# Optimization experiments

Hardware: AMD Instinct MI355X
Metric: run time of the kernel (lower is better)

Reference implementation:

```python
import jax, jax.numpy as jnp
import numpy as np

B, L, D = 2, 2048, 2048
NUM_HEADS = 32
KV_GROUPS = 8
GROUP_SIZE = NUM_HEADS // KV_GROUPS  # 4
HEAD_DIM = D // NUM_HEADS            # 64


def _rope_tables(L, hd):
    # standard RoPE angle tables, duplicated across halves to width hd
    inv_freq = 1.0 / (10000.0 ** (np.arange(0, hd, 2, dtype=np.float32) / hd))
    ang = np.arange(L, dtype=np.float32)[:, None] * inv_freq[None, :]  # [L, hd/2]
    cos = np.concatenate([np.cos(ang), np.cos(ang)], axis=-1)
    sin = np.concatenate([np.sin(ang), np.sin(ang)], axis=-1)
    return jnp.asarray(cos), jnp.asarray(sin)


def setup_inputs() -> dict:
    key = jax.random.key(0)
    ks = jax.random.split(key, 6)
    x = jax.random.normal(ks[0], (B, L, D), dtype=jnp.float32)
    mask = jnp.triu(jnp.ones((L, L), dtype=bool), k=1)  # causal: True above diag
    cos, sin = _rope_tables(L, HEAD_DIM)
    s = 0.02
    Wq = jax.random.normal(ks[1], (D, D), dtype=jnp.float32) * s
    Wk = jax.random.normal(ks[2], (D, KV_GROUPS * HEAD_DIM), dtype=jnp.float32) * s
    Wv = jax.random.normal(ks[3], (D, KV_GROUPS * HEAD_DIM), dtype=jnp.float32) * s
    Wo = jax.random.normal(ks[4], (D, D), dtype=jnp.float32) * s
    bo = jnp.zeros((D,), dtype=jnp.float32)
    return {"x": x, "mask": mask, "cos": cos, "sin": sin,
            "Wq": Wq, "Wk": Wk, "Wv": Wv, "Wo": Wo, "bo": bo}


def _apply_rope(t, cos, sin):
    # t: [B, H, L, hd]
    hd = t.shape[-1]
    t1, t2 = t[..., : hd // 2], t[..., hd // 2:]
    rotated = jnp.concatenate([-t2, t1], axis=-1)
    return t * cos[None, None, :, :] + rotated * sin[None, None, :, :]


def reference(x, mask, cos, sin, Wq, Wk, Wv, Wo, bo):
    Bv, Lv, Dv = x.shape
    hd = HEAD_DIM
    q = (x @ Wq).reshape(Bv, Lv, NUM_HEADS, hd).transpose(0, 2, 1, 3)   # [B,H,L,hd]
    k = (x @ Wk).reshape(Bv, Lv, KV_GROUPS, hd).transpose(0, 2, 1, 3)   # [B,G,L,hd]
    v = (x @ Wv).reshape(Bv, Lv, KV_GROUPS, hd).transpose(0, 2, 1, 3)
    q = _apply_rope(q, cos, sin)
    k = _apply_rope(k, cos, sin)
    k = jnp.repeat(k, GROUP_SIZE, axis=1)  # [B,H,L,hd]
    v = jnp.repeat(v, GROUP_SIZE, axis=1)
    scores = jnp.einsum('bhqd,bhkd->bhqk', q, k) / jnp.sqrt(jnp.float32(hd))
    scores = jnp.where(mask[None, None, :, :], -jnp.inf, scores)
    attn = jax.nn.softmax(scores, axis=-1)
    out = jnp.einsum('bhqk,bhkd->bhqd', attn, v)         # [B,H,L,hd]
    out = out.transpose(0, 2, 1, 3).reshape(Bv, Lv, Dv)  # [B,L,D]
    return out @ Wo + bo
```

## Files before the change

kernel.cpp:

```cpp
#include <hip/hip_runtime.h>
#include <cstdint>

typedef unsigned short UST;
typedef __bf16 v8bf __attribute__((ext_vector_type(8)));
typedef float v4f __attribute__((ext_vector_type(4)));

static __device__ __forceinline__ UST f2b(float f) {
  union { float f; uint32_t u; } c; c.f = f;
  uint32_t u = c.u;
  u += 0x7fffu + ((u >> 16) & 1u);
  return (UST)(u >> 16);
}
static __device__ __forceinline__ float b2f(UST h) {
  union { uint32_t u; float f; } c; c.u = ((uint32_t)h) << 16;
  return c.f;
}
static __device__ __forceinline__ uint32_t cvtpk(float lo, float hi) {
  uint32_t r;
  asm("v_cvt_pk_bf16_f32 %0, %1, %2" : "=v"(r) : "v"(lo), "v"(hi));
  return r;
}
static __device__ __forceinline__ float fexp2(float x) {
  float r;
  asm("v_exp_f32 %0, %1" : "=v"(r) : "v"(x));
  return r;
}
template <int N>
static __device__ __forceinline__ void wait_vm() {
  asm volatile("s_waitcnt vmcnt(%0)" :: "i"(N));
}

static __device__ __forceinline__ void gl_lds16(const UST* g, UST* l) {
  __builtin_amdgcn_global_load_lds(
      (const __attribute__((address_space(1))) void*)g,
      (__attribute__((address_space(3))) void*)l, 16, 0, 0);
}

__global__ __launch_bounds__(256) void k_cast(const float* __restrict__ src,
                                              UST* __restrict__ dst) {
  size_t i = (size_t)blockIdx.x * 256 + threadIdx.x;
  const float4* s4 = reinterpret_cast<const float4*>(src) + 2 * i;
  float4 a = s4[0], b = s4[1];
  union { UST s[8]; uint4 v; } r;
  r.s[0] = f2b(a.x); r.s[1] = f2b(a.y); r.s[2] = f2b(a.z); r.s[3] = f2b(a.w);
  r.s[4] = f2b(b.x); r.s[5] = f2b(b.y); r.s[6] = f2b(b.z); r.s[7] = f2b(b.w);
  reinterpret_cast<uint4*>(dst)[i] = r.v;
}

__global__ __launch_bounds__(256) void k_castT(const float* __restrict__ W,
                                               UST* __restrict__ dst, int N, int K) {
  __shared__ float tile[32][33];
  int nt = blockIdx.x * 32, kt = blockIdx.y * 32;
  int tx = threadIdx.x, ty = threadIdx.y;
#pragma unroll
  for (int r = 0; r < 4; ++r)
    tile[ty + r * 8][tx] = W[(size_t)(kt + ty + r * 8) * N + nt + tx];
  __syncthreads();
#pragma unroll
  for (int r = 0; r < 4; ++r)
    dst[(size_t)(nt + ty + r * 8) * K + kt + tx] = f2b(tile[tx][ty + r * 8]);
}

template <int BM, int BN, int WM, int WN, int EPI>
__global__ __launch_bounds__(512, 2) void k_gemm2(const UST* __restrict__ A,
                                                  const UST* __restrict__ Bt,
                                                  void* __restrict__ Cv,
                                                  const float* __restrict__ bias,
                                                  int M, int N, int K, int ntn) {
  constexpr int WMR = BM / WM, WNR = BN / WN;
  constexpr int MF = WMR / 16, NF = WNR / 16;
  constexpr int CA = BM / 64, CB = BN / 64;
  constexpr int NKEEP = CA + CB;
  constexpr int AE = 2 * BM * 64;
  __shared__ __align__(16) UST lds[AE + 2 * BN * 64];

  int tid = threadIdx.x, w = tid >> 6, lane = tid & 63;
  int lr = lane & 15, lg = lane >> 4;
  int wm = w / WN, wn = w % WN;

  int q = (int)gridDim.x >> 3;
  int bid = (int)blockIdx.x;
  int swz = (bid & 7) * q + (bid >> 3);
  int mBlk = (swz / ntn) * BM, nBlk = (swz % ntn) * BN;

  v4f acc[MF][NF];
#pragma unroll
  for (int i = 0; i < MF; ++i)
#pragma unroll
    for (int j = 0; j < NF; ++j) acc[i][j] = (v4f){0.f, 0.f, 0.f, 0.f};

  int tr = tid >> 3;
  int sg = (tid & 7) ^ (tr & 7);
  const UST* AbL = A + (size_t)(mBlk + tr) * K + sg * 8;
  const UST* BbL = Bt + (size_t)(nBlk + tr) * K + sg * 8;
  int ldsW = w * 512;

  auto stageA = [&](int bf, int kt) {
#pragma unroll
    for (int c = 0; c < CA; ++c)
      gl_lds16(AbL + (size_t)(c * 64) * K + kt * 64,
               &lds[bf * BM * 64 + c * 4096 + ldsW]);
  };
  auto stageB = [&](int bf, int kt) {
#pragma unroll
    for (int c = 0; c < CB; ++c)
      gl_lds16(BbL + (size_t)(c * 64) * K + kt * 64,
               &lds[AE + bf * BN * 64 + c * 4096 + ldsW]);
  };
  auto ldA = [&](int bf, int s, int f) -> v8bf {
    int row = wm * WMR + f * 16 + lr;
    return *(const v8bf*)&lds[(bf * BM + row) * 64 + (((s * 4 + lg) ^ (lr & 7)) * 8)];
  };
  auto ldB = [&](int bf, int s, int nf) -> v8bf {
    int row = wn * WNR + nf * 16 + lr;
    return *(const v8bf*)&lds[AE + (bf * BN + row) * 64 + (((s * 4 + lg) ^ (lr & 7)) * 8)];
  };

  int NT = K >> 6;
  stageA(0, 0); stageB(0, 0);

  for (int kt = 0; kt < NT; ++kt) {
    int bf = kt & 1, nb = bf ^ 1;
    if (kt + 1 < NT) {
      stageA(nb, kt + 1); stageB(nb, kt + 1);
      wait_vm<NKEEP>();
    } else {
      wait_vm<0>();
    }
    __syncthreads();
#pragma unroll
    for (int s = 0; s < 2; ++s) {
      v8bf afr[MF], bfr[NF];
#pragma unroll
      for (int nf = 0; nf < NF; ++nf) bfr[nf] = ldB(bf, s, nf);
#pragma unroll
      for (int f = 0; f < MF; ++f) afr[f] = ldA(bf, s, f);
      __builtin_amdgcn_s_setprio(1);
#pragma unroll
      for (int f = 0; f < MF; ++f)
#pragma unroll
        for (int nf = 0; nf < NF; ++nf)
          acc[f][nf] = __builtin_amdgcn_mfma_f32_16x16x32_bf16(
              afr[f], bfr[nf], acc[f][nf], 0, 0, 0);
      __builtin_amdgcn_s_setprio(0);
    }
    __syncthreads();
  }

  int row0 = mBlk + wm * WMR + lg * 4;
  int col0 = nBlk + wn * WNR + lr;
#pragma unroll
  for (int fm = 0; fm < MF; ++fm)
#pragma unroll
    for (int nf = 0; nf < NF; ++nf)
#pragma unroll
      for (int r = 0; r < 4; ++r) {
        int row = row0 + fm * 16 + r;
        int col = col0 + nf * 16;
        if constexpr (EPI == 0) {
          ((UST*)Cv)[(size_t)row * N + col] = f2b(acc[fm][nf][r]);
        } else {
          ((float*)Cv)[(size_t)row * N + col] = acc[fm][nf][r] + bias[col];
        }
      }
}

__global__ __launch_bounds__(256) void k_rope(const UST* __restrict__ qkv,
                                              const float* __restrict__ cosT,
                                              const float* __restrict__ sinT,
                                              UST* __restrict__ qh,
                                              UST* __restrict__ kh) {
  int idx = blockIdx.x * 256 + threadIdx.x;
  int d = idx & 31;
  int hh = (idx >> 5) % 40;
  int row = idx / 1280;
  int l = row & 2047, b = row >> 11;
  int col = (hh < 32) ? hh * 64 : 2048 + (hh - 32) * 64;
  float t1 = b2f(qkv[(size_t)row * 3072 + col + d]);
  float t2 = b2f(qkv[(size_t)row * 3072 + col + d + 32]);
  float c = cosT[l * 64 + d], s = sinT[l * 64 + d];
  float o1 = t1 * c - t2 * s;
  float o2 = t2 * c + t1 * s;
  if (hh < 32) {
    size_t base = (((size_t)b * 32 + hh) * 2048 + l) * 64 + d;
    qh[base] = f2b(o1 * 0.125f);
    qh[base + 32] = f2b(o2 * 0.125f);
  } else {
    size_t base = (((size_t)b * 8 + (hh - 32)) * 2048 + l) * 64 + d;
    kh[base] = f2b(o1);
    kh[base + 32] = f2b(o2);
  }
}

__global__ __launch_bounds__(256) void k_vtrans(const UST* __restrict__ qkv,
                                                UST* __restrict__ vt) {
  __shared__ __align__(16) UST tl[64][72];
  int lt = blockIdx.x, bg = blockIdx.y;
  int b = bg >> 3, g = bg & 7;
  int t = threadIdx.x;
  int li = t >> 2, d0 = (t & 3) * 16;
  const UST* src = qkv + (size_t)(b * 2048 + lt * 64 + li) * 3072 + 2560 + g * 64 + d0;
  *(uint4*)&tl[li][d0] = *(const uint4*)src;
  *(uint4*)&tl[li][d0 + 8] = *(const uint4*)(src + 8);
  __syncthreads();
  int d = t >> 2, l0 = (t & 3) * 16;
  union { UST u[8]; uint4 v; } r0, r1;
#pragma unroll
  for (int e = 0; e < 8; ++e) r0.u[e] = tl[l0 + e][d];
#pragma unroll
  for (int e = 0; e < 8; ++e) r1.u[e] = tl[l0 + 8 + e][d];
  UST* dstp = vt + (size_t)((b * 8 + g) * 64 + d) * 2048 + (size_t)lt * 64 + l0;
  *(uint4*)dstp = r0.v;
  *(uint4*)(dstp + 8) = r1.v;
}

__global__ __launch_bounds__(512, 4) void k_attn(const UST* __restrict__ qh,
                                                 const UST* __restrict__ kh,
                                                 const UST* __restrict__ vt,
                                                 UST* __restrict__ outp) {
  __shared__ __align__(16) UST k_s[128 * 72];
  __shared__ __align__(16) UST v_s[64 * 136];
  __shared__ __align__(16) UST p_s[8][16 * 136];
  int bx = blockIdx.x, h = blockIdx.y, b = blockIdx.z;
  int g = h >> 2;
  int tid = threadIdx.x, w = tid >> 6, lane = tid & 63;
  int lr = lane & 15, lg = lane >> 4;

  int ksr = tid >> 2, ksc = (tid & 3) * 16;
  int vsr = tid >> 3, vsc = (tid & 7) * 16;
  const UST* kbase = kh + ((size_t)(b * 8 + g) * 2048 + ksr) * 64 + ksc;
  const UST* vbase = vt + ((size_t)(b * 8 + g) * 64 + vsr) * 2048 + vsc;
  UST* kdst = &k_s[ksr * 72 + ksc];
  UST* vdst = &v_s[vsr * 136 + vsc];

  for (int half = 0; half < 2; ++half) {
    int qt = half ? (15 - bx) : bx;
    int qbase = qt * 128 + w * 16;

    const UST* qp = qh + ((size_t)(b * 32 + h) * 2048 + qbase + lr) * 64 + lg * 8;
    v8bf qf0 = *(const v8bf*)qp;
    v8bf qf1 = *(const v8bf*)(qp + 32);

    float m = -1e30f, ls = 0.f;
    v4f o[4];
#pragma unroll
    for (int dt = 0; dt < 4; ++dt) o[dt] = (v4f){0.f, 0.f, 0.f, 0.f};

    __syncthreads();
    uint4 pk0 = *(const uint4*)kbase, pk1 = *(const uint4*)(kbase + 8);
    uint4 pv0 = *(const uint4*)vbase, pv1 = *(const uint4*)(vbase + 8);
    *(uint4*)kdst = pk0; *(uint4*)(kdst + 8) = pk1;
    *(uint4*)vdst = pv0; *(uint4*)(vdst + 8) = pv1;

    for (int j = 0; j <= qt; ++j) {
      __syncthreads();
      bool pref = (j < qt);
      if (pref) {
        const UST* kg = kbase + (size_t)(j + 1) * 8192;
        const UST* vg = vbase + (j + 1) * 128;
        pk0 = *(const uint4*)kg; pk1 = *(const uint4*)(kg + 8);
        pv0 = *(const uint4*)vg; pv1 = *(const uint4*)(vg + 8);
      }

      v4f st[8];
      __builtin_amdgcn_s_setprio(1);
#pragma unroll
      for (int kt = 0; kt < 8; ++kt) {
        const UST* kr = &k_s[(kt * 16 + lr) * 72 + lg * 8];
        v8bf kf0 = *(const v8bf*)kr;
        v8bf kf1 = *(const v8bf*)(kr + 32);
        v4f z = (v4f){0.f, 0.f, 0.f, 0.f};
        z = __builtin_amdgcn_mfma_f32_16x16x32_bf16(kf0, qf0, z, 0, 0, 0);
        z = __builtin_amdgcn_mfma_f32_16x16x32_bf16(kf1, qf1, z, 0, 0, 0);
        st[kt] = z;
      }
      __builtin_amdgcn_s_setprio(0);
      if (j == qt) {
        int qg = qbase + lr;
#pragma unroll
        for (int kt = 0; kt < 8; ++kt)
#pragma unroll
          for (int r = 0; r < 4; ++r) {
            int kg2 = j * 128 + kt * 16 + 4 * lg + r;
            if (kg2 > qg) st[kt][r] = -1e30f;
          }
      }

      float t0 = fmaxf(fmaxf(st[0][0], st[0][1]), fmaxf(st[0][2], st[0][3]));
      float t1 = fmaxf(fmaxf(st[1][0], st[1][1]), fmaxf(st[1][2], st[1][3]));
      float t2 = fmaxf(fmaxf(st[2][0], st[2][1]), fmaxf(st[2][2], st[2][3]));
      float t3 = fmaxf(fmaxf(st[3][0], st[3][1]), fmaxf(st[3][2], st[3][3]));
      float t4 = fmaxf(fmaxf(st[4][0], st[4][1]), fmaxf(st[4][2], st[4][3]));
      float t5 = fmaxf(fmaxf(st[5][0], st[5][1]), fmaxf(st[5][2], st[5][3]));
      float t6 = fmaxf(fmaxf(st[6][0], st[6][1]), fmaxf(st[6][2], st[6][3]));
      float t7 = fmaxf(fmaxf(st[7][0], st[7][1]), fmaxf(st[7][2], st[7][3]));
      float mx = fmaxf(fmaxf(fmaxf(t0, t1), fmaxf(t2, t3)),
                       fmaxf(fmaxf(t4, t5), fmaxf(t6, t7)));
      mx = fmaxf(mx, __shfl_xor(mx, 16));
      mx = fmaxf(mx, __shfl_xor(mx, 32));

      if (!__all(mx <= m + 8.f)) {
        float mn = fmaxf(m, mx);
        float al = __expf(m - mn);
        m = mn;
        ls *= al;
#pragma unroll
        for (int r = 0; r < 4; ++r) {
          float ar = __shfl(al, 4 * lg + r);
          o[0][r] *= ar; o[1][r] *= ar; o[2][r] *= ar; o[3][r] *= ar;
        }
      }

      constexpr float LOG2E = 1.44269504f;
      float mlog = m * LOG2E;
      float rs = 0.f;
      UST* pw = &p_s[w][lr * 136 + 4 * lg];
#pragma unroll
      for (int kt = 0; kt < 8; ++kt) {
        float p0 = fexp2(__builtin_fmaf(st[kt][0], LOG2E, -mlog));
        float p1 = fexp2(__builtin_fmaf(st[kt][1], LOG2E, -mlog));
        float p2 = fexp2(__builtin_fmaf(st[kt][2], LOG2E, -mlog));
        float p3 = fexp2(__builtin_fmaf(st[kt][3], LOG2E, -mlog));
        rs += (p0 + p1) + (p2 + p3);
        uint2 q2;
        q2.x = cvtpk(p0, p1);
        q2.y = cvtpk(p2, p3);
        *(uint2*)(pw + kt * 16) = q2;
      }
      rs += __shfl_xor(rs, 16);
      rs += __shfl_xor(rs, 32);
      ls += rs;

      __builtin_amdgcn_s_setprio(1);
#pragma unroll
      for (int kk = 0; kk < 4; ++kk) {
        v8bf pa = *(const v8bf*)&p_s[w][lr * 136 + kk * 32 + lg * 8];
#pragma unroll
        for (int dt = 0; dt < 4; ++dt) {
          v8bf vb = *(const v8bf*)&v_s[(dt * 16 + lr) * 136 + kk * 32 + lg * 8];
          o[dt] = __builtin_amdgcn_mfma_f32_16x16x32_bf16(pa, vb, o[dt], 0, 0, 0);
        }
      }
      __builtin_amdgcn_s_setprio(0);

      __syncthreads();
      if (pref) {
        *(uint4*)kdst = pk0; *(uint4*)(kdst + 8) = pk1;
        *(uint4*)vdst = pv0; *(uint4*)(vdst + 8) = pv1;
      }
    }

    float iv = 1.f / ls;
#pragma unroll
    for (int r = 0; r < 4; ++r) {
      float ivr = __shfl(iv, 4 * lg + r);
      size_t rowb = ((size_t)b * 2048 + qbase + 4 * lg + r) * 2048 + h * 64 + lr;
#pragma unroll
      for (int dt = 0; dt < 4; ++dt)
        outp[rowb + dt * 16] = f2b(o[dt][r] * ivr);
    }
  }
}

extern "C" void kernel_launch(void* const* d_in, const int* in_sizes, int n_in,
                              void* d_out, int out_size, void* d_ws, size_t ws_size,
                              hipStream_t stream) {
  const float* x    = (const float*)d_in[0];
  const float* cosT = (const float*)d_in[2];
  const float* sinT = (const float*)d_in[3];
  const float* Wq   = (const float*)d_in[4];
  const float* Wk   = (const float*)d_in[5];
  const float* Wv   = (const float*)d_in[6];
  const float* Wo   = (const float*)d_in[7];
  const float* bo   = (const float*)d_in[8];
  float* out = (float*)d_out;

  char* ws = (char*)d_ws;
  UST* xb   = (UST*)(ws);
  UST* wcat = (UST*)(ws + 16777216);
  UST* wot  = (UST*)(ws + 29360128);
  UST* qkv  = (UST*)(ws + 37748736);
  UST* qhp  = (UST*)(ws + 62914560);
  UST* khp  = (UST*)(ws + 79691776);
  UST* vtp  = (UST*)(ws + 83886080);
  UST* attn_o = xb;

  k_cast<<<4096, 256, 0, stream>>>(x, xb);
  k_castT<<<dim3(64, 64), dim3(32, 8), 0, stream>>>(Wq, wcat, 2048, 2048);
  k_castT<<<dim3(16, 64), dim3(32, 8), 0, stream>>>(Wk, wcat + (size_t)2048 * 2048, 512, 2048);
  k_castT<<<dim3(16, 64), dim3(32, 8), 0, stream>>>(Wv, wcat + (size_t)2560 * 2048, 512, 2048);
  k_castT<<<dim3(64, 64), dim3(32, 8), 0, stream>>>(Wo, wot, 2048, 2048);

  k_gemm2<256, 192, 2, 4, 0><<<256, 512, 0, stream>>>(xb, wcat, qkv, nullptr,
                                                      4096, 3072, 2048, 16);
  k_rope<<<20480, 256, 0, stream>>>(qkv, cosT, sinT, qhp, khp);
  k_vtrans<<<dim3(32, 16), 256, 0, stream>>>(qkv, vtp);
  k_attn<<<dim3(8, 32, 2), 512, 0, stream>>>(qhp, khp, vtp, attn_o);
  k_gemm2<256, 128, 4, 2, 1><<<256, 512, 0, stream>>>(attn_o, wot, out, bo,
                                                      4096, 2048, 2048, 16);
}
```

Measured before the change: 218.5 us.

## Split GEMM MFMA phases with wave barriers and vectorize RoPE kernel

Within the GEMM main loop, the A-fragment loads and MFMAs are split into NMH sub-phases, each bracketed by s_barrier. The trailing __syncthreads is replaced by these barriers so waves interleave LDS reads and MFMA work in lockstep (ping-pong style). The QKV GEMM uses two halves and the output GEMM one. The RoPE kernel now handles 8 elements per thread with 128-bit loads and stores instead of scalar bf16 accesses, cutting the thread count eightfold. The extra barriers add synchronization cost, and removing the end-of-iteration __syncthreads leaves the LDS reuse correctness depending on the new barrier placement.

```diff
diff --git a/kernel.cpp b/kernel.cpp
--- a/kernel.cpp
+++ b/kernel.cpp
@@ -61,14 +61,14 @@
     dst[(size_t)(nt + ty + r * 8) * K + kt + tx] = f2b(tile[tx][ty + r * 8]);
 }
 
-template <int BM, int BN, int WM, int WN, int EPI>
+template <int BM, int BN, int WM, int WN, int NMH, int EPI>
 __global__ __launch_bounds__(512, 2) void k_gemm2(const UST* __restrict__ A,
                                                   const UST* __restrict__ Bt,
                                                   void* __restrict__ Cv,
                                                   const float* __restrict__ bias,
                                                   int M, int N, int K, int ntn) {
   constexpr int WMR = BM / WM, WNR = BN / WN;
-  constexpr int MF = WMR / 16, NF = WNR / 16;
+  constexpr int MF = WMR / 16, NF = WNR / 16, MH = MF / NMH;
   constexpr int CA = BM / 64, CB = BN / 64;
   constexpr int NKEEP = CA + CB;
   constexpr int AE = 2 * BM * 64;
@@ -118,6 +118,8 @@
 
   int NT = K >> 6;
   stageA(0, 0); stageB(0, 0);
+  wait_vm<0>();
+  __builtin_amdgcn_s_barrier();
 
   for (int kt = 0; kt < NT; ++kt) {
     int bf = kt & 1, nb = bf ^ 1;
@@ -130,21 +132,28 @@
     __syncthreads();
 #pragma unroll
     for (int s = 0; s < 2; ++s) {
-      v8bf afr[MF], bfr[NF];
-#pragma unroll
-      for (int nf = 0; nf < NF; ++nf) bfr[nf] = ldB(bf, s, nf);
-#pragma unroll
-      for (int f = 0; f < MF; ++f) afr[f] = ldA(bf, s, f);
-      __builtin_amdgcn_s_setprio(1);
-#pragma unroll
-      for (int f = 0; f < MF; ++f)
-#pragma unroll
-        for (int nf = 0; nf < NF; ++nf)
-          acc[f][nf] = __builtin_amdgcn_mfma_f32_16x16x32_bf16(
-              afr[f], bfr[nf], acc[f][nf], 0, 0, 0);
-      __builtin_amdgcn_s_setprio(0);
+      v8bf bfr[NF];
+#pragma unroll
+      for (int mh = 0; mh < NMH; ++mh) {
+        v8bf afr[MH];
+        if (mh == 0) {
+#pragma unroll
+          for (int nf = 0; nf < NF; ++nf) bfr[nf] = ldB(bf, s, nf);
+        }
+#pragma unroll
+        for (int f = 0; f < MH; ++f) afr[f] = ldA(bf, s, mh * MH + f);
+        __builtin_amdgcn_s_barrier();
+        __builtin_amdgcn_s_setprio(1);
+#pragma unroll
+        for (int f = 0; f < MH; ++f)
+#pragma unroll
+          for (int nf = 0; nf < NF; ++nf)
+            acc[mh * MH + f][nf] = __builtin_amdgcn_mfma_f32_16x16x32_bf16(
+                afr[f], bfr[nf], acc[mh * MH + f][nf], 0, 0, 0);
+        __builtin_amdgcn_s_setprio(0);
+        __builtin_amdgcn_s_barrier();
+      }
     }
-    __syncthreads();
   }
 
   int row0 = mBlk + wm * WMR + lg * 4;
@@ -171,25 +180,33 @@
                                               UST* __restrict__ qh,
                                               UST* __restrict__ kh) {
   int idx = blockIdx.x * 256 + threadIdx.x;
-  int d = idx & 31;
-  int hh = (idx >> 5) % 40;
-  int row = idx / 1280;
+  int q4 = idx & 3;
+  int hh = (idx >> 2) % 40;
+  int row = idx / 160;
   int l = row & 2047, b = row >> 11;
+  int d0 = q4 * 8;
   int col = (hh < 32) ? hh * 64 : 2048 + (hh - 32) * 64;
-  float t1 = b2f(qkv[(size_t)row * 3072 + col + d]);
-  float t2 = b2f(qkv[(size_t)row * 3072 + col + d + 32]);
-  float c = cosT[l * 64 + d], s = sinT[l * 64 + d];
-  float o1 = t1 * c - t2 * s;
-  float o2 = t2 * c + t1 * s;
-  if (hh < 32) {
-    size_t base = (((size_t)b * 32 + hh) * 2048 + l) * 64 + d;
-    qh[base] = f2b(o1 * 0.125f);
-    qh[base + 32] = f2b(o2 * 0.125f);
-  } else {
-    size_t base = (((size_t)b * 8 + (hh - 32)) * 2048 + l) * 64 + d;
-    kh[base] = f2b(o1);
-    kh[base + 32] = f2b(o2);
+  const UST* sp = qkv + (size_t)row * 3072 + col + d0;
+  union { uint4 v; UST u[8]; } t1, t2, o1, o2;
+  t1.v = *(const uint4*)sp;
+  t2.v = *(const uint4*)(sp + 32);
+  const float4* cp = (const float4*)&cosT[l * 64 + d0];
+  const float4* sn = (const float4*)&sinT[l * 64 + d0];
+  float4 ca = cp[0], cb = cp[1], sa = sn[0], sb = sn[1];
+  float cc[8] = {ca.x, ca.y, ca.z, ca.w, cb.x, cb.y, cb.z, cb.w};
+  float ss[8] = {sa.x, sa.y, sa.z, sa.w, sb.x, sb.y, sb.z, sb.w};
+  float scale = (hh < 32) ? 0.125f : 1.f;
+#pragma unroll
+  for (int j = 0; j < 8; ++j) {
+    float a = b2f(t1.u[j]), bb = b2f(t2.u[j]);
+    o1.u[j] = f2b((a * cc[j] - bb * ss[j]) * scale);
+    o2.u[j] = f2b((bb * cc[j] + a * ss[j]) * scale);
   }
+  UST* dst = (hh < 32)
+      ? qh + (((size_t)b * 32 + hh) * 2048 + l) * 64 + d0
+      : kh + (((size_t)b * 8 + (hh - 32)) * 2048 + l) * 64 + d0;
+  *(uint4*)dst = o1.v;
+  *(uint4*)(dst + 32) = o2.v;
 }
 
 __global__ __launch_bounds__(256) void k_vtrans(const UST* __restrict__ qkv,
@@ -391,11 +408,11 @@
   k_castT<<<dim3(16, 64), dim3(32, 8), 0, stream>>>(Wv, wcat + (size_t)2560 * 2048, 512, 2048);
   k_castT<<<dim3(64, 64), dim3(32, 8), 0, stream>>>(Wo, wot, 2048, 2048);
 
-  k_gemm2<256, 192, 2, 4, 0><<<256, 512, 0, stream>>>(xb, wcat, qkv, nullptr,
-                                                      4096, 3072, 2048, 16);
-  k_rope<<<20480, 256, 0, stream>>>(qkv, cosT, sinT, qhp, khp);
+  k_gemm2<256, 192, 2, 4, 2, 0><<<256, 512, 0, stream>>>(xb, wcat, qkv, nullptr,
+                                                         4096, 3072, 2048, 16);
+  k_rope<<<2560, 256, 0, stream>>>(qkv, cosT, sinT, qhp, khp);
   k_vtrans<<<dim3(32, 16), 256, 0, stream>>>(qkv, vtp);
   k_attn<<<dim3(8, 32, 2), 512, 0, stream>>>(qhp, khp, vtp, attn_o);
-  k_gemm2<256, 128, 4, 2, 1><<<256, 512, 0, stream>>>(attn_o, wot, out, bo,
-                                                      4096, 2048, 2048, 16);
-}
+  k_gemm2<256, 128, 4, 2, 1, 1><<<256, 512, 0, stream>>>(attn_o, wot, out, bo,
+                                                         4096, 2048, 2048, 16);
+}
```

After: 225.2 us. +3.1%, slower.
